# Performance work log

Measured on AMD Instinct MI355X. Metric: run time of the kernel, lower is better.

Reference implementation:

```python
import jax, jax.numpy as jnp
from jax import lax
import numpy as np
import math

B, T, HID = 4, 2048, 1024
NH, KS, INTER = 8, 4, 2816
HD = HID // NH
CHUNK = 32
EPS = 1e-6


def setup_inputs() -> dict:
    key = jax.random.key(0)
    ks = jax.random.split(key, 16)
    def w(k, shape, fan_in):
        return jax.random.normal(k, shape, jnp.float32) * (1.0 / math.sqrt(fan_in))
    logit = math.log(0.95 / 0.05)
    return {
        'x': jax.random.normal(ks[0], (B, T, HID), jnp.float32),
        'qkv_w': w(ks[1], (3 * HID, HID), HID),
        'out_proj_w': w(ks[2], (HID, HID), HID),
        'out_gate_w': w(ks[3], (HID, HID), HID),
        'out_gate_b': jnp.zeros((HID,), jnp.float32),
        'decay_param': jnp.full((NH,), logit, jnp.float32),
        'conv_w': w(ks[4], (HID, 1, KS), KS),      # depthwise: [out, in/groups=1, k]
        'conv_b': jnp.zeros((HID,), jnp.float32),
        'pw_w': w(ks[5], (HID, HID), HID),
        'gate_w': w(ks[6], (HID, 2 * HID), 2 * HID),
        'w1': w(ks[7], (INTER, HID), HID),
        'w2': w(ks[8], (INTER, HID), HID),
        'w3': w(ks[9], (HID, INTER), INTER),
        'norm1_w': jnp.ones((HID,), jnp.float32),
        'norm2_w': jnp.ones((HID,), jnp.float32),
    }


def rmsnorm(x, w, eps=EPS):
    ms = jnp.mean(jnp.square(x), axis=-1, keepdims=True)
    return x * lax.rsqrt(ms + eps) * w


def decay_scan(x, decay, init):
    # inclusive scan out[t] = decay*out[t-1] + x[t]; x:[B,NH,T,HD], decay:[1,NH,1], init:[B,NH,HD]
    b, h, t, d = x.shape
    c = min(CHUNK, t)
    log_d = jnp.log(jnp.maximum(decay.astype(jnp.float32), 1e-8))        # [1,NH,1]
    idx = jnp.arange(c, dtype=jnp.float32)
    log_p = log_d[..., None] * idx[None, None, :, None]                  # [1,NH,c,1]
    p, inv_p = jnp.exp(log_p), jnp.exp(-log_p)
    init_p = jnp.exp(log_d[..., None] * (idx + 1.0)[None, None, :, None])
    xc = x.astype(jnp.float32).reshape(b, h, t // c, c, d)
    xc = jnp.moveaxis(xc, 2, 0)                                          # [Nc,B,NH,c,HD]
    def step(state, chunk):
        cs = jnp.cumsum(chunk * inv_p, axis=2)
        out = cs * p + state[:, :, None, :] * init_p
        return out[:, :, -1, :], out
    _, outs = lax.scan(step, init.astype(jnp.float32), xc)
    out = jnp.moveaxis(outs, 0, 2).reshape(b, h, t, d)
    return out.astype(x.dtype)


def _forward(x, qkv_w, out_proj_w, out_gate_w, out_gate_b, decay_param,
             conv_w, conv_b, pw_w, gate_w, w1, w2, w3, norm1_w, norm2_w):
    b, t, _ = x.shape
    h = rmsnorm(x, norm1_w)

    # ---- LocalConv (depthwise causal conv + pointwise) ----
    xc = jnp.transpose(h, (0, 2, 1))                                     # [B,HID,T]
    pad = jnp.zeros((b, HID, KS - 1), x.dtype)
    xc = jnp.concatenate([pad, xc], axis=2)
    conv = lax.conv_general_dilated(xc, conv_w, (1,), 'VALID',
                                    dimension_numbers=('NCH', 'OIH', 'NCH'),
                                    feature_group_count=HID)
    conv = conv + conv_b[None, :, None]
    conv = jnp.transpose(conv, (0, 2, 1))                                # [B,T,HID]
    local = jnp.einsum('bth,oh->bto', jax.nn.silu(conv), pw_w)

    # ---- LinearAttention ----
    qkv = jnp.einsum('bth,oh->bto', h, qkv_w)
    q, k, v = jnp.split(qkv, 3, axis=-1)
    def heads(z):
        return jnp.transpose(z.reshape(b, t, NH, HD), (0, 2, 1, 3))      # [B,NH,T,HD]
    q, k, v = heads(q), heads(k), heads(v)
    q = jax.nn.elu(q) + 1.0
    k = jax.nn.elu(k) + 1.0
    decay = jax.nn.sigmoid(decay_param).reshape(1, NH, 1)
    zero_state = jnp.zeros((b, NH, HD), x.dtype)
    running_kv = decay_scan(k * v, decay, zero_state)
    running_ks = decay_scan(k, decay, zero_state)
    den = jnp.maximum(jnp.sum(q * running_ks, axis=-1, keepdims=True), 1e-6)
    o = q * running_kv / den                                             # [B,NH,T,HD]
    v_direct = jnp.transpose(v, (0, 2, 1, 3)).reshape(b, t, HID)
    o = jnp.transpose(o, (0, 2, 1, 3)).reshape(b, t, HID)
    g = jax.nn.sigmoid(jnp.einsum('bth,oh->bto', o, out_gate_w) + out_gate_b)
    o = g * o + (1.0 - g) * v_direct
    attn = jnp.einsum('bth,oh->bto', o, out_proj_w)

    # ---- Gate fusion of local/global, residual ----
    comb = jnp.concatenate([local, attn], axis=-1)
    gmix = jax.nn.sigmoid(jnp.einsum('bth,oh->bto', comb, gate_w))
    x = x + gmix * local + (1.0 - gmix) * attn

    # ---- FFN (SwiGLU) + residual ----
    h2 = rmsnorm(x, norm2_w)
    ffn = jnp.einsum('bti,oi->bto',
                     jax.nn.silu(jnp.einsum('bth,ih->bti', h2, w1)) *
                     jnp.einsum('bth,ih->bti', h2, w2), w3)
    return x + ffn


def reference(x, qkv_w, out_proj_w, out_gate_w, out_gate_b, decay_param,
              conv_w, conv_b, pw_w, gate_w, w1, w2, w3, norm1_w, norm2_w):
    return _forward(x, qkv_w, out_proj_w, out_gate_w, out_gate_b, decay_param,
                    conv_w, conv_b, pw_w, gate_w, w1, w2, w3, norm1_w, norm2_w)
```

## Files before the change

### kernel.cpp

```cpp
#include <hip/hip_runtime.h>
#include <math.h>

static constexpr int Bc    = 4;
static constexpr int Tc    = 2048;
static constexpr int HIDc  = 1024;
static constexpr int NHc   = 8;
static constexpr int HDc   = 128;
static constexpr int Mrows = Bc * Tc;
static constexpr int INTERc= 2816;
static constexpr int CH    = 64;
static constexpr int NC    = Tc / CH;

typedef _Float16 f16;
typedef __attribute__((ext_vector_type(8))) _Float16 f16x8;
typedef __attribute__((ext_vector_type(4))) float f32x4;
typedef unsigned short u16;

union H8 { f16 h[8]; int4 v; u16 u[8]; };
union H4 { f16 h[4]; int2 v; u16 u[4]; };
union F4 { float4 v; float a[4]; };

static __device__ __forceinline__ float sigm(float x) { return 1.0f / (1.0f + expf(-x)); }
static __device__ __forceinline__ float silu(float x) { return x * sigm(x); }
static __device__ __forceinline__ float elu1(float x) { return x > 0.0f ? x + 1.0f : expf(x); }

static __device__ __forceinline__ float h2f(u16 u){ f16 h; __builtin_memcpy(&h,&u,2); return (float)h; }
static __device__ __forceinline__ u16 f2h(float x){ f16 h=(f16)x; u16 u; __builtin_memcpy(&u,&h,2); return u; }
static __device__ __forceinline__ float rec2(u16 h, u16 l){ return h2f(h) + h2f(l); }
static __device__ __forceinline__ void fsplit(float v, u16& h, u16& l){ h = f2h(v); l = f2h(v - h2f(h)); }

static __device__ __forceinline__ void gld16(const u16* g, u16* l)
{
    __builtin_amdgcn_global_load_lds((const __attribute__((address_space(1))) void*)g,
                                     (__attribute__((address_space(3))) void*)l,
                                     16, 0, 0);
}

__global__ __launch_bounds__(256) void wcvt_k(const float* __restrict__ src,
                                              u16* __restrict__ dst, int n8)
{
    const int i = blockIdx.x * 256 + threadIdx.x;
    if (i >= n8) return;
    F4 a, b; a.v = ((const float4*)src)[i * 2]; b.v = ((const float4*)src)[i * 2 + 1];
    H8 o;
    #pragma unroll
    for (int u = 0; u < 4; u++) { o.h[u] = (f16)a.a[u]; o.h[4 + u] = (f16)b.a[u]; }
    ((int4*)dst)[i] = o.v;
}

template<int INPAIR>
__global__ __launch_bounds__(256) void rmsnorm_k(const float* __restrict__ xf,
                                                 const u16* __restrict__ xhi,
                                                 const u16* __restrict__ xlo,
                                                 const float* __restrict__ w,
                                                 u16* __restrict__ ohi,
                                                 u16* __restrict__ olo)
{
    const int row = blockIdx.x;
    const int tid = threadIdx.x;
    const size_t off = (size_t)row * HIDc + tid * 4;
    float xv[4];
    if constexpr (INPAIR) {
        H4 H, L;
        H.v = *(const int2*)(xhi + off);
        L.v = *(const int2*)(xlo + off);
        #pragma unroll
        for (int u = 0; u < 4; u++) xv[u] = (float)H.h[u] + (float)L.h[u];
    } else {
        F4 f; f.v = *(const float4*)(xf + off);
        #pragma unroll
        for (int u = 0; u < 4; u++) xv[u] = f.a[u];
    }
    float ss = xv[0]*xv[0] + xv[1]*xv[1] + xv[2]*xv[2] + xv[3]*xv[3];
    #pragma unroll
    for (int o = 32; o > 0; o >>= 1) ss += __shfl_xor(ss, o);
    __shared__ float sred[4];
    if ((tid & 63) == 0) sred[tid >> 6] = ss;
    __syncthreads();
    const float tot = sred[0] + sred[1] + sred[2] + sred[3];
    const float scale = rsqrtf(tot * (1.0f / (float)HIDc) + 1e-6f);
    F4 wv; wv.v = *(const float4*)(w + tid * 4);
    H4 OH, OL;
    #pragma unroll
    for (int u = 0; u < 4; u++) {
        u16 hh, ll; fsplit(xv[u] * scale * wv.a[u], hh, ll);
        OH.u[u] = hh; OL.u[u] = ll;
    }
    *(int2*)(ohi + off) = OH.v;
    *(int2*)(olo + off) = OL.v;
}

__global__ __launch_bounds__(256) void conv_k(const u16* __restrict__ hhi,
                                              const u16* __restrict__ hlo,
                                              const float* __restrict__ cw,
                                              const float* __restrict__ cb,
                                              u16* __restrict__ ohi,
                                              u16* __restrict__ olo)
{
    const int row = blockIdx.x;
    const int t   = row & (Tc - 1);
    const int ch4 = threadIdx.x * 4;
    const float* wp = cw + (size_t)ch4 * 4;
    F4 bias; bias.v = *(const float4*)(cb + ch4);
    F4 acc;
    #pragma unroll
    for (int u = 0; u < 4; u++) acc.a[u] = bias.a[u];
    #pragma unroll
    for (int j = 0; j < 4; j++) {
        const int tt = t - 3 + j;
        if (tt >= 0) {
            const size_t off = ((size_t)row + j - 3) * HIDc + ch4;
            H4 H, L;
            H.v = *(const int2*)(hhi + off);
            L.v = *(const int2*)(hlo + off);
            #pragma unroll
            for (int u = 0; u < 4; u++) acc.a[u] += ((float)H.h[u] + (float)L.h[u]) * wp[u * 4 + j];
        }
    }
    H4 OH, OL;
    #pragma unroll
    for (int u = 0; u < 4; u++) {
        u16 hh, ll; fsplit(silu(acc.a[u]), hh, ll);
        OH.u[u] = hh; OL.u[u] = ll;
    }
    const size_t off = (size_t)row * HIDc + ch4;
    *(int2*)(ohi + off) = OH.v;
    *(int2*)(olo + off) = OL.v;
}

__global__ __launch_bounds__(64) void scan1_k(u16* __restrict__ khi, u16* __restrict__ klo,
                                              const u16* __restrict__ vhi, const u16* __restrict__ vlo,
                                              u16* __restrict__ shi, u16* __restrict__ slo,
                                              const float* __restrict__ dp)
{
    const int bid = blockIdx.x;
    const int c   = bid & (NC - 1);
    const int bh  = bid >> 5;
    const int b   = bh >> 3, hh = bh & 7;
    const int lane = threadIdx.x;
    const float dec = sigm(dp[hh]);
    const size_t base = (size_t)b * Tc * HIDc + (size_t)(c * CH) * HIDc + hh * HDc + lane * 2;
    float skv0 = 0.f, skv1 = 0.f, sks0 = 0.f, sks1 = 0.f;
    for (int t = 0; t < CH; t++) {
        const size_t p = base + (size_t)t * HIDc;
        const unsigned kh = *(const unsigned*)(khi + p);
        const unsigned kl = *(const unsigned*)(klo + p);
        const unsigned vh = *(const unsigned*)(vhi + p);
        const unsigned vl = *(const unsigned*)(vlo + p);
        const float kx = elu1(rec2((u16)kh, (u16)kl));
        const float ky = elu1(rec2((u16)(kh >> 16), (u16)(kl >> 16)));
        const float vx = rec2((u16)vh, (u16)vl);
        const float vy = rec2((u16)(vh >> 16), (u16)(vl >> 16));
        skv0 = dec * skv0 + kx * vx;
        skv1 = dec * skv1 + ky * vy;
        sks0 = dec * sks0 + kx;
        sks1 = dec * sks1 + ky;
        u16 h0, l0, h1, l1;
        fsplit(skv0, h0, l0); fsplit(skv1, h1, l1);
        *(unsigned*)(khi + p) = (unsigned)h0 | ((unsigned)h1 << 16);
        *(unsigned*)(klo + p) = (unsigned)l0 | ((unsigned)l1 << 16);
        fsplit(sks0, h0, l0); fsplit(sks1, h1, l1);
        *(unsigned*)(shi + p) = (unsigned)h0 | ((unsigned)h1 << 16);
        *(unsigned*)(slo + p) = (unsigned)l0 | ((unsigned)l1 << 16);
    }
}

__global__ __launch_bounds__(64) void scan2_k(u16* __restrict__ qhi, u16* __restrict__ qlo,
                                              const u16* __restrict__ skvhi, const u16* __restrict__ skvlo,
                                              const u16* __restrict__ skshi, const u16* __restrict__ skslo,
                                              const float* __restrict__ dp)
{
    const int bid = blockIdx.x;
    const int c   = bid & (NC - 1);
    const int bh  = bid >> 5;
    const int b   = bh >> 3, hh = bh & 7;
    const int lane = threadIdx.x;
    const float dec = sigm(dp[hh]);
    float dCH = dec;
    #pragma unroll
    for (int i = 0; i < 6; i++) dCH *= dCH;
    const size_t rowbase = (size_t)b * Tc * HIDc + hh * HDc + lane * 2;

    float ckv0 = 0.f, ckv1 = 0.f, cks0 = 0.f, cks1 = 0.f;
    for (int j = 0; j < c; j++) {
        const size_t p = rowbase + (size_t)(j * CH + CH - 1) * HIDc;
        const unsigned ah = *(const unsigned*)(skvhi + p);
        const unsigned al = *(const unsigned*)(skvlo + p);
        const unsigned bh2 = *(const unsigned*)(skshi + p);
        const unsigned bl2 = *(const unsigned*)(skslo + p);
        ckv0 = ckv0 * dCH + rec2((u16)ah, (u16)al);
        ckv1 = ckv1 * dCH + rec2((u16)(ah >> 16), (u16)(al >> 16));
        cks0 = cks0 * dCH + rec2((u16)bh2, (u16)bl2);
        cks1 = cks1 * dCH + rec2((u16)(bh2 >> 16), (u16)(bl2 >> 16));
    }

    const size_t cbase = rowbase + (size_t)(c * CH) * HIDc;
    float pw = dec;
    for (int t = 0; t < CH; t++) {
        const size_t p = cbase + (size_t)t * HIDc;
        const unsigned qh = *(const unsigned*)(qhi + p);
        const unsigned ql = *(const unsigned*)(qlo + p);
        const unsigned ah = *(const unsigned*)(skvhi + p);
        const unsigned al = *(const unsigned*)(skvlo + p);
        const unsigned bh2 = *(const unsigned*)(skshi + p);
        const unsigned bl2 = *(const unsigned*)(skslo + p);
        const float qx = elu1(rec2((u16)qh, (u16)ql));
        const float qy = elu1(rec2((u16)(qh >> 16), (u16)(ql >> 16)));
        const float skv0 = rec2((u16)ah, (u16)al) + pw * ckv0;
        const float skv1 = rec2((u16)(ah >> 16), (u16)(al >> 16)) + pw * ckv1;
        const float sks0 = rec2((u16)bh2, (u16)bl2) + pw * cks0;
        const float sks1 = rec2((u16)(bh2 >> 16), (u16)(bl2 >> 16)) + pw * cks1;
        float part = qx * sks0 + qy * sks1;
        #pragma unroll
        for (int o = 32; o > 0; o >>= 1) part += __shfl_xor(part, o);
        const float inv = 1.0f / fmaxf(part, 1e-6f);
        u16 h0, l0, h1, l1;
        fsplit(qx * skv0 * inv, h0, l0);
        fsplit(qy * skv1 * inv, h1, l1);
        *(unsigned*)(qhi + p) = (unsigned)h0 | ((unsigned)h1 << 16);
        *(unsigned*)(qlo + p) = (unsigned)l0 | ((unsigned)l1 << 16);
        pw *= dec;
    }
}

template<int MODE, int PRE>
__global__ __launch_bounds__(256) void gemm_f16_k(
    const u16* __restrict__ Ahi, const u16* __restrict__ Alo,
    const u16* __restrict__ A2hi, const u16* __restrict__ A2lo, int lda,
    const u16* __restrict__ Wh, const float* __restrict__ Wf,
    float* __restrict__ Cout,
    u16* __restrict__ Chi, u16* __restrict__ Clo, int ldc,
    int K, int kSplit, int nx,
    const float* __restrict__ bias,
    const float* __restrict__ E0f,
    const u16* __restrict__ E0hi, const u16* __restrict__ E0lo, int ldE0,
    const u16* __restrict__ E1hi, const u16* __restrict__ E1lo, int ldE1,
    const u16* __restrict__ E2hi, const u16* __restrict__ E2lo, int ldE2)
{
    __shared__ __align__(16) u16 Ah[8][128][8];
    __shared__ __align__(16) u16 Al[8][128][8];
    __shared__ __align__(16) u16 Bs[8][128][8];

    const int tid  = threadIdx.x;
    const int lane = tid & 63;
    const int wv   = tid >> 6;
    const int wr   = wv >> 1, wc = wv & 1;
    const int lr   = lane & 15, lk = lane >> 4;

    const int cpx = gridDim.x >> 3;
    int bid = blockIdx.x;
    bid = (bid & 7) * cpx + (bid >> 3);
    const int n0 = (bid % nx) * 128;
    const int m0 = (bid / nx) * 128;

    f32x4 acc[4][4];
    #pragma unroll
    for (int i = 0; i < 4; i++)
        #pragma unroll
        for (int j = 0; j < 4; j++)
            acc[i][j] = (f32x4){0.f, 0.f, 0.f, 0.f};

    for (int k0 = 0; k0 < K; k0 += 64) {
        const u16* ah = Ahi; const u16* al = Alo; int kb = k0;
        if constexpr (MODE == 4) {
            if (k0 >= kSplit) { ah = A2hi; al = A2lo; kb = k0 - kSplit; }
        }
        F4 wreg[8];
        if constexpr (!PRE) {
            #pragma unroll
            for (int q = 0; q < 2; q++) {
                const float* wp0 = Wf + (size_t)(n0 + lane) * K + k0 + (2 * wv + q) * 8;
                const float* wp1 = wp0 + (size_t)64 * K;
                wreg[q * 4 + 0].v = *(const float4*)(wp0);
                wreg[q * 4 + 1].v = *(const float4*)(wp0 + 4);
                wreg[q * 4 + 2].v = *(const float4*)(wp1);
                wreg[q * 4 + 3].v = *(const float4*)(wp1 + 4);
            }
        }
        __syncthreads();
        #pragma unroll
        for (int q = 0; q < 2; q++) {
            const int cc = 2 * wv + q;
            const size_t a0 = (size_t)(m0 + lane) * lda + kb + cc * 8;
            gld16(ah + a0, &Ah[cc][0][0]);
            gld16(ah + a0 + (size_t)64 * lda, &Ah[cc][64][0]);
            gld16(al + a0, &Al[cc][0][0]);
            gld16(al + a0 + (size_t)64 * lda, &Al[cc][64][0]);
            if constexpr (PRE) {
                const size_t w0 = (size_t)(n0 + lane) * K + k0 + cc * 8;
                gld16(Wh + w0, &Bs[cc][0][0]);
                gld16(Wh + w0 + (size_t)64 * K, &Bs[cc][64][0]);
            } else {
                H8 W0, W1;
                #pragma unroll
                for (int e = 0; e < 8; e++) {
                    W0.h[e] = (f16)wreg[q * 4 + (e >> 2)].a[e & 3];
                    W1.h[e] = (f16)wreg[q * 4 + 2 + (e >> 2)].a[e & 3];
                }
                *(int4*)&Bs[cc][lane][0]      = W0.v;
                *(int4*)&Bs[cc][64 + lane][0] = W1.v;
            }
        }
        __syncthreads();
        #pragma unroll
        for (int ks = 0; ks < 2; ks++) {
            const int ck = ks * 4 + lk;
            f16x8 av[4], au[4], bv[4];
            #pragma unroll
            for (int fi = 0; fi < 4; fi++) {
                av[fi] = *(const f16x8*)&Ah[ck][wr * 64 + fi * 16 + lr][0];
                au[fi] = *(const f16x8*)&Al[ck][wr * 64 + fi * 16 + lr][0];
                bv[fi] = *(const f16x8*)&Bs[ck][wc * 64 + fi * 16 + lr][0];
            }
            #pragma unroll
            for (int i = 0; i < 4; i++)
                #pragma unroll
                for (int j = 0; j < 4; j++) {
                    acc[i][j] = __builtin_amdgcn_mfma_f32_16x16x32_f16(av[i], bv[j], acc[i][j], 0, 0, 0);
                    acc[i][j] = __builtin_amdgcn_mfma_f32_16x16x32_f16(au[i], bv[j], acc[i][j], 0, 0, 0);
                }
        }
    }

    u16* dsth = Chi; u16* dstl = Clo;
    int nbase = n0;
    if constexpr (MODE == 5) {
        const int plane = n0 >> 10;
        nbase = n0 & 1023;
        if (plane == 1)      { dsth = const_cast<u16*>(E0hi); dstl = const_cast<u16*>(E0lo); }
        else if (plane == 2) { dsth = const_cast<u16*>(E1hi); dstl = const_cast<u16*>(E1lo); }
    }
    #pragma unroll
    for (int i = 0; i < 4; i++) {
        #pragma unroll
        for (int j = 0; j < 4; j++) {
            #pragma unroll
            for (int v = 0; v < 4; v++) {
                const size_t r = (size_t)(m0 + wr * 64 + i * 16 + lk * 4 + v);
                const int c = nbase + wc * 64 + j * 16 + lr;
                const size_t idx = r * (size_t)ldc + c;
                float val = acc[i][j][v];
                if constexpr (MODE == 1) {
                    val = silu(val);
                } else if constexpr (MODE == 2) {
                    val = rec2(Chi[idx], Clo[idx]) * val;
                } else if constexpr (MODE == 3) {
                    const float g = sigm(val + bias[c]);
                    const size_t i0 = r * (size_t)ldE0 + c, i1 = r * (size_t)ldE1 + c;
                    val = g * rec2(E0hi[i0], E0lo[i0]) + (1.0f - g) * rec2(E1hi[i1], E1lo[i1]);
                } else if constexpr (MODE == 4) {
                    const float g = sigm(val);
                    const size_t i1 = r * (size_t)ldE1 + c, i2 = r * (size_t)ldE2 + c;
                    val = E0f[r * (size_t)ldE0 + c] + g * rec2(E1hi[i1], E1lo[i1])
                          + (1.0f - g) * rec2(E2hi[i2], E2lo[i2]);
                } else if constexpr (MODE == 6) {
                    Cout[idx] = rec2(Chi[idx], Clo[idx]) + val;
                    continue;
                }
                u16 hh, ll; fsplit(val, hh, ll);
                dsth[idx] = hh; dstl[idx] = ll;
            }
        }
    }
}

__global__ __launch_bounds__(256) void gemm_dual_k(
    const u16* __restrict__ Ahi, const u16* __restrict__ Alo, int lda,
    const u16* __restrict__ W1h, const u16* __restrict__ W2h,
    u16* __restrict__ Chi, u16* __restrict__ Clo, int ldc,
    int K, int nx)
{
    __shared__ __align__(16) u16 Ah[8][128][8];
    __shared__ __align__(16) u16 Al[8][128][8];
    __shared__ __align__(16) u16 B1[8][128][8];
    __shared__ __align__(16) u16 B2[8][128][8];

    const int tid  = threadIdx.x;
    const int lane = tid & 63;
    const int wv   = tid >> 6;
    const int wr   = wv >> 1, wc = wv & 1;
    const int lr   = lane & 15, lk = lane >> 4;

    const int cpx = gridDim.x >> 3;
    int bid = blockIdx.x;
    bid = (bid & 7) * cpx + (bid >> 3);
    const int n0 = (bid % nx) * 128;
    const int m0 = (bid / nx) * 128;

    f32x4 acc1[4][4], acc2[4][4];
    #pragma unroll
    for (int i = 0; i < 4; i++)
        #pragma unroll
        for (int j = 0; j < 4; j++) {
            acc1[i][j] = (f32x4){0.f, 0.f, 0.f, 0.f};
            acc2[i][j] = (f32x4){0.f, 0.f, 0.f, 0.f};
        }

    for (int k0 = 0; k0 < K; k0 += 64) {
        __syncthreads();
        #pragma unroll
        for (int q = 0; q < 2; q++) {
            const int cc = 2 * wv + q;
            const size_t a0 = (size_t)(m0 + lane) * lda + k0 + cc * 8;
            gld16(Ahi + a0, &Ah[cc][0][0]);
            gld16(Ahi + a0 + (size_t)64 * lda, &Ah[cc][64][0]);
            gld16(Alo + a0, &Al[cc][0][0]);
            gld16(Alo + a0 + (size_t)64 * lda, &Al[cc][64][0]);
            const size_t w0 = (size_t)(n0 + lane) * K + k0 + cc * 8;
            gld16(W1h + w0, &B1[cc][0][0]);
            gld16(W1h + w0 + (size_t)64 * K, &B1[cc][64][0]);
            gld16(W2h + w0, &B2[cc][0][0]);
            gld16(W2h + w0 + (size_t)64 * K, &B2[cc][64][0]);
        }
        __syncthreads();
        #pragma unroll
        for (int ks = 0; ks < 2; ks++) {
            const int ck = ks * 4 + lk;
            f16x8 av[4], au[4], b1[4], b2[4];
            #pragma unroll
            for (int fi = 0; fi < 4; fi++) {
                av[fi] = *(const f16x8*)&Ah[ck][wr * 64 + fi * 16 + lr][0];
                au[fi] = *(const f16x8*)&Al[ck][wr * 64 + fi * 16 + lr][0];
                b1[fi] = *(const f16x8*)&B1[ck][wc * 64 + fi * 16 + lr][0];
                b2[fi] = *(const f16x8*)&B2[ck][wc * 64 + fi * 16 + lr][0];
            }
            #pragma unroll
            for (int i = 0; i < 4; i++)
                #pragma unroll
                for (int j = 0; j < 4; j++) {
                    acc1[i][j] = __builtin_amdgcn_mfma_f32_16x16x32_f16(av[i], b1[j], acc1[i][j], 0, 0, 0);
                    acc1[i][j] = __builtin_amdgcn_mfma_f32_16x16x32_f16(au[i], b1[j], acc1[i][j], 0, 0, 0);
                    acc2[i][j] = __builtin_amdgcn_mfma_f32_16x16x32_f16(av[i], b2[j], acc2[i][j], 0, 0, 0);
                    acc2[i][j] = __builtin_amdgcn_mfma_f32_16x16x32_f16(au[i], b2[j], acc2[i][j], 0, 0, 0);
                }
        }
    }

    #pragma unroll
    for (int i = 0; i < 4; i++) {
        #pragma unroll
        for (int j = 0; j < 4; j++) {
            #pragma unroll
            for (int v = 0; v < 4; v++) {
                const size_t r = (size_t)(m0 + wr * 64 + i * 16 + lk * 4 + v);
                const int c = n0 + wc * 64 + j * 16 + lr;
                const size_t idx = r * (size_t)ldc + c;
                const float val = silu(acc1[i][j][v]) * acc2[i][j][v];
                u16 hh, ll; fsplit(val, hh, ll);
                Chi[idx] = hh; Clo[idx] = ll;
            }
        }
    }
}

template<int MODE>
static inline void launch_gemm(bool pre, int nblocks, int nx, hipStream_t stream,
    const u16* Ahi, const u16* Alo, const u16* A2hi, const u16* A2lo, int lda,
    const u16* Wh, const float* Wf,
    float* Cout, u16* Chi, u16* Clo, int ldc, int K, int kSplit,
    const float* bias, const float* E0f,
    const u16* E0hi, const u16* E0lo, int ldE0,
    const u16* E1hi, const u16* E1lo, int ldE1,
    const u16* E2hi, const u16* E2lo, int ldE2)
{
    if (pre)
        gemm_f16_k<MODE, 1><<<dim3(nblocks), dim3(256), 0, stream>>>(Ahi, Alo, A2hi, A2lo, lda, Wh, Wf,
            Cout, Chi, Clo, ldc, K, kSplit, nx, bias, E0f, E0hi, E0lo, ldE0, E1hi, E1lo, ldE1, E2hi, E2lo, ldE2);
    else
        gemm_f16_k<MODE, 0><<<dim3(nblocks), dim3(256), 0, stream>>>(Ahi, Alo, A2hi, A2lo, lda, Wh, Wf,
            Cout, Chi, Clo, ldc, K, kSplit, nx, bias, E0f, E0hi, E0lo, ldE0, E1hi, E1lo, ldE1, E2hi, E2lo, ldE2);
}

extern "C" void kernel_launch(void* const* d_in, const int* in_sizes, int n_in,
                              void* d_out, int out_size, void* d_ws, size_t ws_size,
                              hipStream_t stream)
{
    const float* x           = (const float*)d_in[0];
    const float* qkv_w       = (const float*)d_in[1];
    const float* out_proj_w  = (const float*)d_in[2];
    const float* out_gate_w  = (const float*)d_in[3];
    const float* out_gate_b  = (const float*)d_in[4];
    const float* decay_param = (const float*)d_in[5];
    const float* conv_w      = (const float*)d_in[6];
    const float* conv_b      = (const float*)d_in[7];
    const float* pw_w        = (const float*)d_in[8];
    const float* gate_w      = (const float*)d_in[9];
    const float* w1          = (const float*)d_in[10];
    const float* w2          = (const float*)d_in[11];
    const float* w3          = (const float*)d_in[12];
    const float* norm1_w     = (const float*)d_in[13];
    const float* norm2_w     = (const float*)d_in[14];
    float* OUT = (float*)d_out;

    float* ws = (float*)d_ws;
    const size_t S8 = (size_t)Mrows * HIDc;
    u16* P0h = (u16*)(ws + 0 * S8); u16* P0l = P0h + S8;
    u16* P1h = (u16*)(ws + 1 * S8); u16* P1l = P1h + S8;
    u16* P2h = (u16*)(ws + 2 * S8); u16* P2l = P2h + S8;
    u16* P3h = (u16*)(ws + 3 * S8); u16* P3l = P3h + S8;
    u16* OUTh = (u16*)OUT;          u16* OUTl = OUTh + S8;
    u16* T1h = P1h;                 u16* T1l = P1h + (size_t)Mrows * INTERc;

    constexpr size_t SZ_QKV  = (size_t)3 * HIDc * HIDc;
    constexpr size_t SZ_SQ   = (size_t)HIDc * HIDc;
    constexpr size_t SZ_GATE = (size_t)2 * HIDc * HIDc;
    constexpr size_t SZ_W1   = (size_t)INTERc * HIDc;
    constexpr size_t W_ELEMS = SZ_QKV + 3 * SZ_SQ + SZ_GATE + 3 * SZ_W1;
    const bool pre = (ws_size >= 4 * S8 * sizeof(float) + W_ELEMS * sizeof(u16));

    u16* wb   = (u16*)(ws + 4 * S8);
    u16* qkvH = wb;
    u16* pwH  = qkvH + SZ_QKV;
    u16* ogH  = pwH  + SZ_SQ;
    u16* opH  = ogH  + SZ_SQ;
    u16* gaH  = opH  + SZ_SQ;
    u16* w1H  = gaH  + SZ_GATE;
    u16* w2H  = w1H  + SZ_W1;
    u16* w3H  = w2H  + SZ_W1;

    const dim3 blk(256);
    const int nb8  = 8 * (Mrows / 128);
    const int nb22 = 22 * (Mrows / 128);
    const int nb24 = 24 * (Mrows / 128);
    const u16* nu = nullptr;

    if (pre) {
        wcvt_k<<<(int)(SZ_QKV / 8 / 256), blk, 0, stream>>>(qkv_w, qkvH, (int)(SZ_QKV / 8));
        wcvt_k<<<(int)(SZ_SQ  / 8 / 256), blk, 0, stream>>>(pw_w,  pwH,  (int)(SZ_SQ  / 8));
        wcvt_k<<<(int)(SZ_SQ  / 8 / 256), blk, 0, stream>>>(out_gate_w, ogH, (int)(SZ_SQ / 8));
        wcvt_k<<<(int)(SZ_SQ  / 8 / 256), blk, 0, stream>>>(out_proj_w, opH, (int)(SZ_SQ / 8));
        wcvt_k<<<(int)(SZ_GATE/ 8 / 256), blk, 0, stream>>>(gate_w, gaH, (int)(SZ_GATE / 8));
        wcvt_k<<<(int)(SZ_W1  / 8 / 256), blk, 0, stream>>>(w1, w1H, (int)(SZ_W1 / 8));
        wcvt_k<<<(int)(SZ_W1  / 8 / 256), blk, 0, stream>>>(w2, w2H, (int)(SZ_W1 / 8));
        wcvt_k<<<(int)(SZ_W1  / 8 / 256), blk, 0, stream>>>(w3, w3H, (int)(SZ_W1 / 8));
    }

    rmsnorm_k<0><<<Mrows, blk, 0, stream>>>(x, nullptr, nullptr, norm1_w, P0h, P0l);
    conv_k<<<Mrows, blk, 0, stream>>>(P0h, P0l, conv_w, conv_b, P1h, P1l);
    launch_gemm<0>(pre, nb8, 8, stream, P1h, P1l, nu, nu, HIDc, pwH, pw_w,
                   nullptr, P2h, P2l, HIDc, HIDc, 0, nullptr, nullptr,
                   nu, nu, 0, nu, nu, 0, nu, nu, 0);
    if (pre) {
        launch_gemm<5>(pre, nb24, 24, stream, P0h, P0l, nu, nu, HIDc, qkvH, qkv_w,
                       nullptr, P1h, P1l, HIDc, HIDc, 0, nullptr, nullptr,
                       P3h, P3l, HIDc, OUTh, OUTl, HIDc, nu, nu, 0);
    } else {
        launch_gemm<0>(pre, nb8, 8, stream, P0h, P0l, nu, nu, HIDc, qkvH, qkv_w,
                       nullptr, P1h, P1l, HIDc, HIDc, 0, nullptr, nullptr,
                       nu, nu, 0, nu, nu, 0, nu, nu, 0);
        launch_gemm<0>(pre, nb8, 8, stream, P0h, P0l, nu, nu, HIDc, qkvH + SZ_SQ, qkv_w + SZ_SQ,
                       nullptr, P3h, P3l, HIDc, HIDc, 0, nullptr, nullptr,
                       nu, nu, 0, nu, nu, 0, nu, nu, 0);
        launch_gemm<0>(pre, nb8, 8, stream, P0h, P0l, nu, nu, HIDc, qkvH + 2 * SZ_SQ, qkv_w + 2 * SZ_SQ,
                       nullptr, OUTh, OUTl, HIDc, HIDc, 0, nullptr, nullptr,
                       nu, nu, 0, nu, nu, 0, nu, nu, 0);
    }
    scan1_k<<<Bc * NHc * NC, dim3(64), 0, stream>>>(P3h, P3l, OUTh, OUTl, P0h, P0l, decay_param);
    scan2_k<<<Bc * NHc * NC, dim3(64), 0, stream>>>(P1h, P1l, P3h, P3l, P0h, P0l, decay_param);
    launch_gemm<3>(pre, nb8, 8, stream, P1h, P1l, nu, nu, HIDc, ogH, out_gate_w,
                   nullptr, P0h, P0l, HIDc, HIDc, 0, out_gate_b, nullptr,
                   P1h, P1l, HIDc, OUTh, OUTl, HIDc, nu, nu, 0);
    launch_gemm<0>(pre, nb8, 8, stream, P0h, P0l, nu, nu, HIDc, opH, out_proj_w,
                   nullptr, P3h, P3l, HIDc, HIDc, 0, nullptr, nullptr,
                   nu, nu, 0, nu, nu, 0, nu, nu, 0);
    launch_gemm<4>(pre, nb8, 8, stream, P2h, P2l, P3h, P3l, HIDc, gaH, gate_w,
                   nullptr, P0h, P0l, HIDc, 2 * HIDc, HIDc, nullptr, x,
                   nu, nu, HIDc, P2h, P2l, HIDc, P3h, P3l, HIDc);
    rmsnorm_k<1><<<Mrows, blk, 0, stream>>>(nullptr, P0h, P0l, norm2_w, OUTh, OUTl);
    if (pre) {
        gemm_dual_k<<<dim3(nb22), blk, 0, stream>>>(OUTh, OUTl, HIDc, w1H, w2H,
                                                    T1h, T1l, INTERc, HIDc, 22);
    } else {
        launch_gemm<1>(pre, nb22, 22, stream, OUTh, OUTl, nu, nu, HIDc, w1H, w1,
                       nullptr, T1h, T1l, INTERc, HIDc, 0, nullptr, nullptr,
                       nu, nu, 0, nu, nu, 0, nu, nu, 0);
        launch_gemm<2>(pre, nb22, 22, stream, OUTh, OUTl, nu, nu, HIDc, w2H, w2,
                       nullptr, T1h, T1l, INTERc, HIDc, 0, nullptr, nullptr,
                       nu, nu, 0, nu, nu, 0, nu, nu, 0);
    }
    launch_gemm<6>(pre, nb8, 8, stream, T1h, T1l, nu, nu, INTERc, w3H, w3,
                   OUT, P0h, P0l, HIDc, INTERc, 0, nullptr, nullptr,
                   nu, nu, 0, nu, nu, 0, nu, nu, 0);
}
```

Before: 1.324 ms.

## Overlap next K-tile loads with MFMA compute in GEMM kernels

```diff
diff --git a/kernel.cpp b/kernel.cpp
--- a/kernel.cpp
+++ b/kernel.cpp
@@ -237,9 +237,9 @@
     const u16* __restrict__ E1hi, const u16* __restrict__ E1lo, int ldE1,
     const u16* __restrict__ E2hi, const u16* __restrict__ E2lo, int ldE2)
 {
-    __shared__ __align__(16) u16 Ah[8][128][8];
-    __shared__ __align__(16) u16 Al[8][128][8];
-    __shared__ __align__(16) u16 Bs[8][128][8];
+    __shared__ __align__(16) u16 Ah[4][128][8];
+    __shared__ __align__(16) u16 Al[4][128][8];
+    __shared__ __align__(16) u16 Bs[4][128][8];
 
     const int tid  = threadIdx.x;
     const int lane = tid & 63;
@@ -260,66 +260,63 @@
         for (int j = 0; j < 4; j++)
             acc[i][j] = (f32x4){0.f, 0.f, 0.f, 0.f};
 
-    for (int k0 = 0; k0 < K; k0 += 64) {
+    auto stage = [&](int t) {
+        const int k0 = t * 32;
         const u16* ah = Ahi; const u16* al = Alo; int kb = k0;
         if constexpr (MODE == 4) {
             if (k0 >= kSplit) { ah = A2hi; al = A2lo; kb = k0 - kSplit; }
         }
-        F4 wreg[8];
-        if constexpr (!PRE) {
+        const size_t a0 = (size_t)(m0 + lane) * lda + kb + wv * 8;
+        gld16(ah + a0, &Ah[wv][0][0]);
+        gld16(ah + a0 + (size_t)64 * lda, &Ah[wv][64][0]);
+        gld16(al + a0, &Al[wv][0][0]);
+        gld16(al + a0 + (size_t)64 * lda, &Al[wv][64][0]);
+        if constexpr (PRE) {
+            const size_t w0 = (size_t)(n0 + lane) * K + k0 + wv * 8;
+            gld16(Wh + w0, &Bs[wv][0][0]);
+            gld16(Wh + w0 + (size_t)64 * K, &Bs[wv][64][0]);
+        } else {
+            const float* wp0 = Wf + (size_t)(n0 + lane) * K + k0 + wv * 8;
+            const float* wp1 = wp0 + (size_t)64 * K;
+            F4 g0, g1, g2, g3;
+            g0.v = *(const float4*)(wp0); g1.v = *(const float4*)(wp0 + 4);
+            g2.v = *(const float4*)(wp1); g3.v = *(const float4*)(wp1 + 4);
+            H8 W0, W1;
             #pragma unroll
-            for (int q = 0; q < 2; q++) {
-                const float* wp0 = Wf + (size_t)(n0 + lane) * K + k0 + (2 * wv + q) * 8;
-                const float* wp1 = wp0 + (size_t)64 * K;
-                wreg[q * 4 + 0].v = *(const float4*)(wp0);
-                wreg[q * 4 + 1].v = *(const float4*)(wp0 + 4);
-                wreg[q * 4 + 2].v = *(const float4*)(wp1);
-                wreg[q * 4 + 3].v = *(const float4*)(wp1 + 4);
+            for (int e = 0; e < 4; e++) {
+                W0.h[e] = (f16)g0.a[e]; W0.h[4 + e] = (f16)g1.a[e];
+                W1.h[e] = (f16)g2.a[e]; W1.h[4 + e] = (f16)g3.a[e];
             }
+            *(int4*)&Bs[wv][lane][0]      = W0.v;
+            *(int4*)&Bs[wv][64 + lane][0] = W1.v;
+        }
+    };
+
+    const int NT = K / 32;
+    stage(0);
+    __syncthreads();
+
+    for (int t = 0; ; ) {
+        f16x8 av[4], au[4], bv[4];
+        #pragma unroll
+        for (int fi = 0; fi < 4; fi++) {
+            av[fi] = *(const f16x8*)&Ah[lk][wr * 64 + fi * 16 + lr][0];
+            au[fi] = *(const f16x8*)&Al[lk][wr * 64 + fi * 16 + lr][0];
+            bv[fi] = *(const f16x8*)&Bs[lk][wc * 64 + fi * 16 + lr][0];
         }
         __syncthreads();
-        #pragma unroll
-        for (int q = 0; q < 2; q++) {
-            const int cc = 2 * wv + q;
-            const size_t a0 = (size_t)(m0 + lane) * lda + kb + cc * 8;
-            gld16(ah + a0, &Ah[cc][0][0]);
-            gld16(ah + a0 + (size_t)64 * lda, &Ah[cc][64][0]);
-            gld16(al + a0, &Al[cc][0][0]);
-            gld16(al + a0 + (size_t)64 * lda, &Al[cc][64][0]);
-            if constexpr (PRE) {
-                const size_t w0 = (size_t)(n0 + lane) * K + k0 + cc * 8;
-                gld16(Wh + w0, &Bs[cc][0][0]);
-                gld16(Wh + w0 + (size_t)64 * K, &Bs[cc][64][0]);
-            } else {
-                H8 W0, W1;
-                #pragma unroll
-                for (int e = 0; e < 8; e++) {
-                    W0.h[e] = (f16)wreg[q * 4 + (e >> 2)].a[e & 3];
-                    W1.h[e] = (f16)wreg[q * 4 + 2 + (e >> 2)].a[e & 3];
-                }
-                *(int4*)&Bs[cc][lane][0]      = W0.v;
-                *(int4*)&Bs[cc][64 + lane][0] = W1.v;
+        const bool more = (t + 1 < NT);
+        if (more) stage(t + 1);
+        #pragma unroll
+        for (int i = 0; i < 4; i++)
+            #pragma unroll
+            for (int j = 0; j < 4; j++) {
+                acc[i][j] = __builtin_amdgcn_mfma_f32_16x16x32_f16(av[i], bv[j], acc[i][j], 0, 0, 0);
+                acc[i][j] = __builtin_amdgcn_mfma_f32_16x16x32_f16(au[i], bv[j], acc[i][j], 0, 0, 0);
             }
-        }
+        if (!more) break;
         __syncthreads();
-        #pragma unroll
-        for (int ks = 0; ks < 2; ks++) {
-            const int ck = ks * 4 + lk;
-            f16x8 av[4], au[4], bv[4];
-            #pragma unroll
-            for (int fi = 0; fi < 4; fi++) {
-                av[fi] = *(const f16x8*)&Ah[ck][wr * 64 + fi * 16 + lr][0];
-                au[fi] = *(const f16x8*)&Al[ck][wr * 64 + fi * 16 + lr][0];
-                bv[fi] = *(const f16x8*)&Bs[ck][wc * 64 + fi * 16 + lr][0];
-            }
-            #pragma unroll
-            for (int i = 0; i < 4; i++)
-                #pragma unroll
-                for (int j = 0; j < 4; j++) {
-                    acc[i][j] = __builtin_amdgcn_mfma_f32_16x16x32_f16(av[i], bv[j], acc[i][j], 0, 0, 0);
-                    acc[i][j] = __builtin_amdgcn_mfma_f32_16x16x32_f16(au[i], bv[j], acc[i][j], 0, 0, 0);
-                }
-        }
+        ++t;
     }
 
     u16* dsth = Chi; u16* dstl = Clo;
@@ -370,10 +367,10 @@
     u16* __restrict__ Chi, u16* __restrict__ Clo, int ldc,
     int K, int nx)
 {
-    __shared__ __align__(16) u16 Ah[8][128][8];
-    __shared__ __align__(16) u16 Al[8][128][8];
-    __shared__ __align__(16) u16 B1[8][128][8];
-    __shared__ __align__(16) u16 B2[8][128][8];
+    __shared__ __align__(16) u16 Ah[4][128][8];
+    __shared__ __align__(16) u16 Al[4][128][8];
+    __shared__ __align__(16) u16 B1[4][128][8];
+    __shared__ __align__(16) u16 B2[4][128][8];
 
     const int tid  = threadIdx.x;
     const int lane = tid & 63;
@@ -396,44 +393,48 @@
             acc2[i][j] = (f32x4){0.f, 0.f, 0.f, 0.f};
         }
 
-    for (int k0 = 0; k0 < K; k0 += 64) {
+    auto stage = [&](int t) {
+        const int k0 = t * 32;
+        const size_t a0 = (size_t)(m0 + lane) * lda + k0 + wv * 8;
+        gld16(Ahi + a0, &Ah[wv][0][0]);
+        gld16(Ahi + a0 + (size_t)64 * lda, &Ah[wv][64][0]);
+        gld16(Alo + a0, &Al[wv][0][0]);
+        gld16(Alo + a0 + (size_t)64 * lda, &Al[wv][64][0]);
+        const size_t w0 = (size_t)(n0 + lane) * K + k0 + wv * 8;
+        gld16(W1h + w0, &B1[wv][0][0]);
+        gld16(W1h + w0 + (size_t)64 * K, &B1[wv][64][0]);
+        gld16(W2h + w0, &B2[wv][0][0]);
+        gld16(W2h + w0 + (size_t)64 * K, &B2[wv][64][0]);
+    };
+
+    const int NT = K / 32;
+    stage(0);
+    __syncthreads();
+
+    for (int t = 0; ; ) {
+        f16x8 av[4], au[4], b1[4], b2[4];
+        #pragma unroll
+        for (int fi = 0; fi < 4; fi++) {
+            av[fi] = *(const f16x8*)&Ah[lk][wr * 64 + fi * 16 + lr][0];
+            au[fi] = *(const f16x8*)&Al[lk][wr * 64 + fi * 16 + lr][0];
+            b1[fi] = *(const f16x8*)&B1[lk][wc * 64 + fi * 16 + lr][0];
+            b2[fi] = *(const f16x8*)&B2[lk][wc * 64 + fi * 16 + lr][0];
+        }
         __syncthreads();
-        #pragma unroll
-        for (int q = 0; q < 2; q++) {
-            const int cc = 2 * wv + q;
-            const size_t a0 = (size_t)(m0 + lane) * lda + k0 + cc * 8;
-            gld16(Ahi + a0, &Ah[cc][0][0]);
-            gld16(Ahi + a0 + (size_t)64 * lda, &Ah[cc][64][0]);
-            gld16(Alo + a0, &Al[cc][0][0]);
-            gld16(Alo + a0 + (size_t)64 * lda, &Al[cc][64][0]);
-            const size_t w0 = (size_t)(n0 + lane) * K + k0 + cc * 8;
-            gld16(W1h + w0, &B1[cc][0][0]);
-            gld16(W1h + w0 + (size_t)64 * K, &B1[cc][64][0]);
-            gld16(W2h + w0, &B2[cc][0][0]);
-            gld16(W2h + w0 + (size_t)64 * K, &B2[cc][64][0]);
-        }
+        const bool more = (t + 1 < NT);
+        if (more) stage(t + 1);
+        #pragma unroll
+        for (int i = 0; i < 4; i++)
+            #pragma unroll
+            for (int j = 0; j < 4; j++) {
+                acc1[i][j] = __builtin_amdgcn_mfma_f32_16x16x32_f16(av[i], b1[j], acc1[i][j], 0, 0, 0);
+                acc1[i][j] = __builtin_amdgcn_mfma_f32_16x16x32_f16(au[i], b1[j], acc1[i][j], 0, 0, 0);
+                acc2[i][j] = __builtin_amdgcn_mfma_f32_16x16x32_f16(av[i], b2[j], acc2[i][j], 0, 0, 0);
+                acc2[i][j] = __builtin_amdgcn_mfma_f32_16x16x32_f16(au[i], b2[j], acc2[i][j], 0, 0, 0);
+            }
+        if (!more) break;
         __syncthreads();
-        #pragma unroll
-        for (int ks = 0; ks < 2; ks++) {
-            const int ck = ks * 4 + lk;
-            f16x8 av[4], au[4], b1[4], b2[4];
-            #pragma unroll
-            for (int fi = 0; fi < 4; fi++) {
-                av[fi] = *(const f16x8*)&Ah[ck][wr * 64 + fi * 16 + lr][0];
-                au[fi] = *(const f16x8*)&Al[ck][wr * 64 + fi * 16 + lr][0];
-                b1[fi] = *(const f16x8*)&B1[ck][wc * 64 + fi * 16 + lr][0];
-                b2[fi] = *(const f16x8*)&B2[ck][wc * 64 + fi * 16 + lr][0];
-            }
-            #pragma unroll
-            for (int i = 0; i < 4; i++)
-                #pragma unroll
-                for (int j = 0; j < 4; j++) {
-                    acc1[i][j] = __builtin_amdgcn_mfma_f32_16x16x32_f16(av[i], b1[j], acc1[i][j], 0, 0, 0);
-                    acc1[i][j] = __builtin_amdgcn_mfma_f32_16x16x32_f16(au[i], b1[j], acc1[i][j], 0, 0, 0);
-                    acc2[i][j] = __builtin_amdgcn_mfma_f32_16x16x32_f16(av[i], b2[j], acc2[i][j], 0, 0, 0);
-                    acc2[i][j] = __builtin_amdgcn_mfma_f32_16x16x32_f16(au[i], b2[j], acc2[i][j], 0, 0, 0);
-                }
-        }
+        ++t;
     }
 
     #pragma unroll
```

After: 1.363 ms. +2.9%, slower.
